# Performance work log

Hardware: AMD Instinct MI355X
Metric: run time of the kernel (lower is better)

The kernel has to match this reference:

```python
import jax, jax.numpy as jnp
import numpy as np

B, T, C = 1024, 512, 48

def setup_inputs() -> dict:
    key = jax.random.key(0)
    k1, k2, k3 = jax.random.split(key, 3)
    potentials = jax.random.normal(k1, (B, T, C), dtype=jnp.float32)
    sequence_lengths = jax.random.randint(k2, (B, 1), 1, T).astype(jnp.int32)
    # layer weight: uniform initializer (keras default uniform is U[-0.05, 0.05])
    transitions = jax.random.uniform(k3, (C, C), dtype=jnp.float32, minval=-0.05, maxval=0.05)
    return {"potentials": potentials, "sequence_lengths": sequence_lengths, "transitions": transitions}

def reference(potentials, sequence_lengths, transitions):
    # Faithful jax port of tf.contrib.crf.crf_decode (Viterbi max-plus DP),
    # followed by one_hot as in CRFLayer.call (inference branch of in_train_phase).
    Bb, Tt, Cc = potentials.shape
    seq_len = sequence_lengths.reshape(-1)  # K.flatten

    def fwd_step(score, xs):
        # score: [B,C] viterbi scores at step t-1
        pot_t, t = xs
        total = score[:, :, None] + transitions[None]  # [B, C_prev, C_cur]
        bp = jnp.argmax(total, axis=1).astype(jnp.int32)  # [B,C] best prev tag
        new_score = jnp.max(total, axis=1) + pot_t        # [B,C]
        valid = (t < seq_len)[:, None]                    # mask steps past seq_len
        score = jnp.where(valid, new_score, score)
        bp = jnp.where(valid, bp, jnp.arange(Cc, dtype=jnp.int32)[None])
        return score, bp

    init = potentials[:, 0]                               # [B,C]
    xs = (jnp.swapaxes(potentials[:, 1:], 0, 1), jnp.arange(1, Tt))
    last_score, bps = jax.lax.scan(fwd_step, init, xs)    # bps: [T-1,B,C]

    last_tag = jnp.argmax(last_score, axis=-1).astype(jnp.int32)  # [B]

    def back_step(tag_next, bp):
        prev = jnp.take_along_axis(bp, tag_next[:, None], axis=1)[:, 0]
        return prev, tag_next

    first_tag, tags_rest = jax.lax.scan(back_step, last_tag, bps, reverse=True)
    tags = jnp.concatenate([first_tag[None], tags_rest], axis=0)  # [T,B]
    tags = jnp.swapaxes(tags, 0, 1)                               # [B,T]
    return jax.nn.one_hot(tags, Cc, dtype=potentials.dtype)       # [B,T,C]
```

## Files before the change

### kernel.cpp

```cpp
#include <hip/hip_runtime.h>

#define T_DIM 512
#define C_DIM 48
#define BPS   48
#define CH    4

#if __has_builtin(__builtin_amdgcn_readlane)
#define READLANE_I(v, l) __builtin_amdgcn_readlane((v), (l))
#else
#define READLANE_I(v, l) __shfl((v), (l), 64)
#endif

#if __has_builtin(__builtin_amdgcn_wave_barrier)
#define WAVE_SYNC() do { __asm__ __volatile__("" ::: "memory"); __builtin_amdgcn_wave_barrier(); } while (0)
#else
#define WAVE_SYNC() __asm__ __volatile__("" ::: "memory")
#endif

#define DPP_MAX_STEP(V_, CTRL_) do {                                          \
    int o_ = __builtin_amdgcn_update_dpp(__float_as_int(V_),                  \
                                         __float_as_int(V_),                  \
                                         (CTRL_), 0xF, 0xF, false);           \
    V_ = fmaxf(V_, __int_as_float(o_));                                       \
} while (0)

__device__ __forceinline__ float wave_max_f(float v) {
    DPP_MAX_STEP(v, 0x111);
    DPP_MAX_STEP(v, 0x112);
    DPP_MAX_STEP(v, 0x114);
    DPP_MAX_STEP(v, 0x118);
    DPP_MAX_STEP(v, 0x142);
    DPP_MAX_STEP(v, 0x143);
    return __int_as_float(READLANE_I(__float_as_int(v), 63));
}

__global__ __launch_bounds__(64) void crf_viterbi(
    const float* __restrict__ pot,
    const int*   __restrict__ seqlen,
    const float* __restrict__ trans,
    float*       __restrict__ out)
{
    const int b   = blockIdx.x;
    const int tid = threadIdx.x;
    const int jj  = (tid < C_DIM) ? tid : (C_DIM - 1);

    __shared__ __align__(16) float trl[C_DIM * C_DIM];
    __shared__ unsigned char bp[T_DIM * BPS];
    __shared__ __align__(4) unsigned char tags[T_DIM];
    __shared__ __align__(16) float fsc[64];

    const float* potb = pot + (size_t)b * (T_DIM * C_DIM);
    const int L   = seqlen[b];
    const int thi = L - 1;

    float tm = 0.0f;
    for (int i = tid; i < C_DIM * C_DIM; i += 64) {
        float v = trans[i];
        trl[i] = v;
        tm = fmaxf(tm, fabsf(v));
    }
    const float tmax = wave_max_f(tm);
    const float nC5 = -(5.0f * tmax + 1e-3f);
    const float nC2 = -(2.0f * tmax + 1e-3f);
    WAVE_SYNC();

    float ns = potb[jj];
    float vthr = wave_max_f(ns) + nC2;

    const float* pp = potb + jj;

    float pb[CH];
    float pmr5[CH];
#pragma unroll
    for (int k = 0; k < CH; ++k) {
        int tt = 1 + k; if (tt > T_DIM - 1) tt = T_DIM - 1;
        pb[k] = pp[tt * C_DIM];
    }
#pragma unroll
    for (int k = 0; k < CH; ++k) pmr5[k] = wave_max_f(pb[k]) + nC5;

    for (int t0 = 1; t0 < L; t0 += CH) {
        float nb[CH];
#pragma unroll
        for (int k = 0; k < CH; ++k) {
            int tt = t0 + CH + k; if (tt > T_DIM - 1) tt = T_DIM - 1;
            nb[k] = pp[tt * C_DIM];
        }
#pragma unroll
        for (int k = 0; k < CH; ++k) {
            const int t = t0 + k;
            if (t >= L) break;
            unsigned long long mm =
                __ballot(ns >= vthr) & 0x0000FFFFFFFFFFFFull;
            if (!mm) mm = 0x0000FFFFFFFFFFFFull;
            const int c0 = (int)__builtin_ctzll(mm);
            const unsigned long long m1 = mm & (mm - 1);
            const int c1 = m1 ? (int)__builtin_ctzll(m1) : c0;
            const unsigned long long m2 = m1 & (m1 - 1);
            const int c2 = m2 ? (int)__builtin_ctzll(m2) : c1;
            const unsigned long long m3 = m2 & (m2 - 1);
            const int c3 = m3 ? (int)__builtin_ctzll(m3) : c2;
            unsigned long long rest = m3 & (m3 - 1);
            const float s0 = __int_as_float(READLANE_I(__float_as_int(ns), c0));
            const float s1 = __int_as_float(READLANE_I(__float_as_int(ns), c1));
            const float s2 = __int_as_float(READLANE_I(__float_as_int(ns), c2));
            const float s3 = __int_as_float(READLANE_I(__float_as_int(ns), c3));
            const float g0 = trl[c0 * C_DIM + jj];
            const float g1 = trl[c1 * C_DIM + jj];
            const float g2 = trl[c2 * C_DIM + jj];
            const float g3 = trl[c3 * C_DIM + jj];
            const float v0 = s0 + g0;
            const float v1 = s1 + g1;
            const float v2 = s2 + g2;
            const float v3 = s3 + g3;
            float mx = v0; int wi = c0;
            if (v1 > mx) { mx = v1; wi = c1; }
            if (v2 > mx) { mx = v2; wi = c2; }
            if (v3 > mx) { mx = v3; wi = c3; }
            while (rest) {
                int c = (int)__builtin_ctzll(rest); rest &= rest - 1;
                float s = __int_as_float(READLANE_I(__float_as_int(ns), c));
                float cv = s + trl[c * C_DIM + jj];
                if (cv > mx) { mx = cv; wi = c; }
            }
            bp[t * BPS + tid] = (unsigned char)wi;
            ns   = mx + pb[k];
            vthr = mx + pmr5[k];
        }
        float pmn5[CH];
#pragma unroll
        for (int k = 0; k < CH; ++k) pmn5[k] = wave_max_f(nb[k]) + nC5;
#pragma unroll
        for (int k = 0; k < CH; ++k) { pb[k] = nb[k]; pmr5[k] = pmn5[k]; }
    }

    fsc[tid] = ns;
    WAVE_SYNC();
    __syncthreads();

    const float* fs = fsc;
    float bv = fs[0];
    int   bi = 0;
#pragma unroll
    for (int i = 1; i < C_DIM; ++i) {
        float v = fs[i];
        if (v > bv) { bv = v; bi = i; }
    }
    const int last_tag = __builtin_amdgcn_readfirstlane(bi);

    for (int t = L + tid; t < T_DIM; t += 64) tags[t] = (unsigned char)last_tag;

    int y = last_tag;
    for (int c0 = (thi >> 6) << 6; c0 >= 0; c0 -= 64) {
        int row[64];
#pragma unroll
        for (int k = 0; k < 64; ++k) row[k] = bp[(c0 + k) * BPS + jj];

        int vacc = 0;
#pragma unroll
        for (int k = 63; k >= 0; --k) {
            const int t = c0 + k;
            vacc = (tid == k) ? y : vacc;
            const int ynew = READLANE_I(row[k], y);
            if ((unsigned)(t - 1) < (unsigned)thi) y = ynew;
        }
        const int tk = c0 + tid;
        if (tk <= thi) tags[tk] = (unsigned char)(vacc & 0xff);
    }
    __syncthreads();

    if (tid < C_DIM) {
        const int r = tid / 12;
        const int q = tid - r * 12;
        const int cbase = q * 4;
        float* ob = out + (size_t)b * (T_DIM * C_DIM);
        for (int t0 = 0; t0 < T_DIM; t0 += 4) {
            const unsigned int tg4 = *(const unsigned int*)&tags[t0];
            const int mytag = (int)((tg4 >> (r * 8)) & 0xffu);
            float4 v;
            v.x = (cbase + 0 == mytag) ? 1.0f : 0.0f;
            v.y = (cbase + 1 == mytag) ? 1.0f : 0.0f;
            v.z = (cbase + 2 == mytag) ? 1.0f : 0.0f;
            v.w = (cbase + 3 == mytag) ? 1.0f : 0.0f;
            *(float4*)(ob + (size_t)(t0 + r) * C_DIM + cbase) = v;
        }
    }
}

extern "C" void kernel_launch(void* const* d_in, const int* in_sizes, int n_in,
                              void* d_out, int out_size, void* d_ws, size_t ws_size,
                              hipStream_t stream) {
    const float* pot    = (const float*)d_in[0];
    const int*   sl     = (const int*)d_in[1];
    const float* trans  = (const float*)d_in[2];
    float*       out    = (float*)d_out;
    const int B = in_sizes[1];
    crf_viterbi<<<B, 64, 0, stream>>>(pot, sl, trans, out);
}
```

Baseline: 308.5 us.

## Precompute Viterbi candidate masks from potentials ahead of the recurrence

```diff
diff --git a/kernel.cpp b/kernel.cpp
--- a/kernel.cpp
+++ b/kernel.cpp
@@ -17,21 +17,35 @@
 #define WAVE_SYNC() __asm__ __volatile__("" ::: "memory")
 #endif
 
-#define DPP_MAX_STEP(V_, CTRL_) do {                                          \
-    int o_ = __builtin_amdgcn_update_dpp(__float_as_int(V_),                  \
-                                         __float_as_int(V_),                  \
-                                         (CTRL_), 0xF, 0xF, false);           \
-    V_ = fmaxf(V_, __int_as_float(o_));                                       \
+__device__ __forceinline__ float rlane_f(float x, int lane) {
+    return __int_as_float(READLANE_I(__float_as_int(x), lane));
+}
+
+__device__ __forceinline__ void wave_max4(float& a, float& b, float& c, float& d) {
+#define STEP4(CTRL) do {                                                           \
+    int oa = __builtin_amdgcn_update_dpp(__float_as_int(a), __float_as_int(a),     \
+                                         (CTRL), 0xF, 0xF, false);                 \
+    int ob = __builtin_amdgcn_update_dpp(__float_as_int(b), __float_as_int(b),     \
+                                         (CTRL), 0xF, 0xF, false);                 \
+    int oc = __builtin_amdgcn_update_dpp(__float_as_int(c), __float_as_int(c),     \
+                                         (CTRL), 0xF, 0xF, false);                 \
+    int od = __builtin_amdgcn_update_dpp(__float_as_int(d), __float_as_int(d),     \
+                                         (CTRL), 0xF, 0xF, false);                 \
+    a = fmaxf(a, __int_as_float(oa)); b = fmaxf(b, __int_as_float(ob));            \
+    c = fmaxf(c, __int_as_float(oc)); d = fmaxf(d, __int_as_float(od));            \
 } while (0)
+    STEP4(0x111); STEP4(0x112); STEP4(0x114); STEP4(0x118); STEP4(0x142); STEP4(0x143);
+#undef STEP4
+    a = __int_as_float(READLANE_I(__float_as_int(a), 63));
+    b = __int_as_float(READLANE_I(__float_as_int(b), 63));
+    c = __int_as_float(READLANE_I(__float_as_int(c), 63));
+    d = __int_as_float(READLANE_I(__float_as_int(d), 63));
+}
 
 __device__ __forceinline__ float wave_max_f(float v) {
-    DPP_MAX_STEP(v, 0x111);
-    DPP_MAX_STEP(v, 0x112);
-    DPP_MAX_STEP(v, 0x114);
-    DPP_MAX_STEP(v, 0x118);
-    DPP_MAX_STEP(v, 0x142);
-    DPP_MAX_STEP(v, 0x143);
-    return __int_as_float(READLANE_I(__float_as_int(v), 63));
+    float x = v, y = v, z = v, w = v;
+    wave_max4(x, y, z, w);
+    return x;
 }
 
 __global__ __launch_bounds__(64) void crf_viterbi(
@@ -60,24 +74,20 @@
         tm = fmaxf(tm, fabsf(v));
     }
     const float tmax = wave_max_f(tm);
-    const float nC5 = -(5.0f * tmax + 1e-3f);
-    const float nC2 = -(2.0f * tmax + 1e-3f);
+    const float nC4 = -(4.0f * tmax + 1e-3f);
     WAVE_SYNC();
 
-    float ns = potb[jj];
-    float vthr = wave_max_f(ns) + nC2;
+    float ns   = potb[jj];
+    float prow = ns;
 
     const float* pp = potb + jj;
 
     float pb[CH];
-    float pmr5[CH];
 #pragma unroll
     for (int k = 0; k < CH; ++k) {
         int tt = 1 + k; if (tt > T_DIM - 1) tt = T_DIM - 1;
         pb[k] = pp[tt * C_DIM];
     }
-#pragma unroll
-    for (int k = 0; k < CH; ++k) pmr5[k] = wave_max_f(pb[k]) + nC5;
 
     for (int t0 = 1; t0 < L; t0 += CH) {
         float nb[CH];
@@ -86,12 +96,22 @@
             int tt = t0 + CH + k; if (tt > T_DIM - 1) tt = T_DIM - 1;
             nb[k] = pp[tt * C_DIM];
         }
+
+        float r0 = prow, r1 = pb[0], r2 = pb[1], r3 = pb[2];
+        float p0 = r0, p1 = r1, p2 = r2, p3 = r3;
+        wave_max4(p0, p1, p2, p3);
+        unsigned long long mk[CH];
+        mk[0] = __ballot(r0 >= p0 + nC4) & 0x0000FFFFFFFFFFFFull;
+        mk[1] = __ballot(r1 >= p1 + nC4) & 0x0000FFFFFFFFFFFFull;
+        mk[2] = __ballot(r2 >= p2 + nC4) & 0x0000FFFFFFFFFFFFull;
+        mk[3] = __ballot(r3 >= p3 + nC4) & 0x0000FFFFFFFFFFFFull;
+        int ca[CH], cb[CH], cc[CH], cd[CH];
+        bool h3[CH];
+        unsigned long long rest[CH];
+        float ga[CH], gb[CH], gc[CH], gd[CH];
 #pragma unroll
         for (int k = 0; k < CH; ++k) {
-            const int t = t0 + k;
-            if (t >= L) break;
-            unsigned long long mm =
-                __ballot(ns >= vthr) & 0x0000FFFFFFFFFFFFull;
+            unsigned long long mm = mk[k];
             if (!mm) mm = 0x0000FFFFFFFFFFFFull;
             const int c0 = (int)__builtin_ctzll(mm);
             const unsigned long long m1 = mm & (mm - 1);
@@ -100,38 +120,46 @@
             const int c2 = m2 ? (int)__builtin_ctzll(m2) : c1;
             const unsigned long long m3 = m2 & (m2 - 1);
             const int c3 = m3 ? (int)__builtin_ctzll(m3) : c2;
-            unsigned long long rest = m3 & (m3 - 1);
-            const float s0 = __int_as_float(READLANE_I(__float_as_int(ns), c0));
-            const float s1 = __int_as_float(READLANE_I(__float_as_int(ns), c1));
-            const float s2 = __int_as_float(READLANE_I(__float_as_int(ns), c2));
-            const float s3 = __int_as_float(READLANE_I(__float_as_int(ns), c3));
-            const float g0 = trl[c0 * C_DIM + jj];
-            const float g1 = trl[c1 * C_DIM + jj];
-            const float g2 = trl[c2 * C_DIM + jj];
-            const float g3 = trl[c3 * C_DIM + jj];
-            const float v0 = s0 + g0;
-            const float v1 = s1 + g1;
-            const float v2 = s2 + g2;
-            const float v3 = s3 + g3;
-            float mx = v0; int wi = c0;
-            if (v1 > mx) { mx = v1; wi = c1; }
-            if (v2 > mx) { mx = v2; wi = c2; }
-            if (v3 > mx) { mx = v3; wi = c3; }
-            while (rest) {
-                int c = (int)__builtin_ctzll(rest); rest &= rest - 1;
-                float s = __int_as_float(READLANE_I(__float_as_int(ns), c));
+            ca[k] = c0; cb[k] = c1; cc[k] = c2; cd[k] = c3;
+            h3[k] = (m2 != 0);
+            rest[k] = m3 & (m3 - 1);
+            ga[k] = trl[c0 * C_DIM + jj];
+            gb[k] = trl[c1 * C_DIM + jj];
+            gc[k] = trl[c2 * C_DIM + jj];
+            gd[k] = trl[c3 * C_DIM + jj];
+        }
+
+#pragma unroll
+        for (int k = 0; k < CH; ++k) {
+            const int t = t0 + k;
+            if (t >= L) break;
+            const float sa = rlane_f(ns, ca[k]);
+            const float sb = rlane_f(ns, cb[k]);
+            const float va = sa + ga[k];
+            const float vb = sb + gb[k];
+            float mx = va; int wi = ca[k];
+            if (vb > va) { mx = vb; wi = cb[k]; }
+            if (h3[k]) {
+                const float sc_ = rlane_f(ns, cc[k]);
+                const float sd_ = rlane_f(ns, cd[k]);
+                const float vc = sc_ + gc[k];
+                const float vd = sd_ + gd[k];
+                if (vc > mx) { mx = vc; wi = cc[k]; }
+                if (vd > mx) { mx = vd; wi = cd[k]; }
+            }
+            unsigned long long rr = rest[k];
+            while (rr) {
+                int c = (int)__builtin_ctzll(rr); rr &= rr - 1;
+                float s = rlane_f(ns, c);
                 float cv = s + trl[c * C_DIM + jj];
                 if (cv > mx) { mx = cv; wi = c; }
             }
             bp[t * BPS + tid] = (unsigned char)wi;
-            ns   = mx + pb[k];
-            vthr = mx + pmr5[k];
-        }
-        float pmn5[CH];
-#pragma unroll
-        for (int k = 0; k < CH; ++k) pmn5[k] = wave_max_f(nb[k]) + nC5;
-#pragma unroll
-        for (int k = 0; k < CH; ++k) { pb[k] = nb[k]; pmr5[k] = pmn5[k]; }
+            ns = mx + pb[k];
+        }
+        prow = pb[CH - 1];
+#pragma unroll
+        for (int k = 0; k < CH; ++k) pb[k] = nb[k];
     }
 
     fsc[tid] = ns;
```

After: 289.1 us. -6.3%, faster.
